# Kernel optimization log

Measured on AMD Instinct MI355X. Metric: run time of the kernel, lower is better.

Reference implementation:

```python
import jax, jax.numpy as jnp
import numpy as np

B, S, V, H, L, NH, DH, F, T = 256, 64, 21128, 768, 12, 12, 64, 3072, 11


def _layernorm(x, g, b):
    m = x.mean(-1, keepdims=True)
    v = ((x - m) ** 2).mean(-1, keepdims=True)
    return (x - m) / jnp.sqrt(v + 1e-12) * g + b


def setup_inputs():
    key = jax.random.key(0)
    ks = iter(jax.random.split(key, 24))
    std = 0.02
    w = lambda shape: jax.random.normal(next(ks), shape, jnp.float32) * std
    return {
        "input_ids": jax.random.randint(next(ks), (B, S), 0, V),
        "attention_mask": jnp.ones((B, S), jnp.int32),
        "label": jax.random.randint(next(ks), (B, S), 0, T),
        "word_emb": w((V, H)),
        "pos_emb": w((S, H)),
        "tok_emb": w((2, H)),
        "emb_ln_g": jnp.ones((H,), jnp.float32),
        "emb_ln_b": jnp.zeros((H,), jnp.float32),
        "Wqkv": w((L, H, 3 * H)),
        "bqkv": jnp.zeros((L, 3 * H), jnp.float32),
        "Wo": w((L, H, H)),
        "bo": jnp.zeros((L, H), jnp.float32),
        "ln1_g": jnp.ones((L, H), jnp.float32),
        "ln1_b": jnp.zeros((L, H), jnp.float32),
        "W1": w((L, H, F)),
        "b1": jnp.zeros((L, F), jnp.float32),
        "W2": w((L, F, H)),
        "b2": jnp.zeros((L, H), jnp.float32),
        "ln2_g": jnp.ones((L, H), jnp.float32),
        "ln2_b": jnp.zeros((L, H), jnp.float32),
        "fc_w": w((H, T)),
        "fc_b": jnp.zeros((T,), jnp.float32),
        "crf_start": w((T,)),
        "crf_end": w((T,)),
        "crf_trans": w((T, T)),
    }


def _encode(ids, mask, word_emb, pos_emb, tok_emb, eg, eb, layer_params):
    x = word_emb[ids] + pos_emb[None] + tok_emb[0][None, None]  # [B,S,H]
    x = _layernorm(x, eg, eb)
    bias = (1.0 - mask.astype(x.dtype))[:, None, None, :] * -1e9  # [B,1,1,S]

    def layer(x, p):
        Wqkv, bqkv, Wo, bo, g1, b1n, W1, b1, W2, b2, g2, b2n = p
        q, k, v = jnp.split(x @ Wqkv + bqkv, 3, axis=-1)
        sh = lambda t: t.reshape(B, S, NH, DH).transpose(0, 2, 1, 3)
        att = jax.nn.softmax(
            jnp.einsum("bhqd,bhkd->bhqk", sh(q), sh(k)) / jnp.sqrt(jnp.float32(DH)) + bias, -1
        )
        o = jnp.einsum("bhqk,bhkd->bhqd", att, sh(v)).transpose(0, 2, 1, 3).reshape(B, S, H)
        x = _layernorm(x + o @ Wo + bo, g1, b1n)
        h = jax.nn.gelu(x @ W1 + b1)
        x = _layernorm(x + h @ W2 + b2, g2, b2n)
        return x, None

    x, _ = jax.lax.scan(layer, x, layer_params)
    return x


def _crf_llh(em, tags, maskf, start, end, trans):
    # torchcrf log-likelihood, batch_first. em:[B,S,T] tags:[B,S] maskf:[B,S]
    bidx = jnp.arange(B)
    score = start[tags[:, 0]] + em[bidx, 0, tags[:, 0]]

    def num_step(s, xs):
        e_t, tp, tc, m = xs
        return s + (trans[tp, tc] + e_t[bidx, tc]) * m, None

    score, _ = jax.lax.scan(
        num_step, score,
        (em[:, 1:].transpose(1, 0, 2), tags[:, :-1].T, tags[:, 1:].T, maskf[:, 1:].T),
    )
    last_idx = maskf.sum(-1).astype(jnp.int32) - 1
    score = score + end[tags[bidx, last_idx]]

    alpha = start[None] + em[:, 0]  # [B,T]

    def den_step(a, xs):
        e_t, m = xs
        nxt = jax.scipy.special.logsumexp(a[:, :, None] + trans[None] + e_t[:, None, :], axis=1)
        return jnp.where(m[:, None] > 0, nxt, a), None

    alpha, _ = jax.lax.scan(den_step, alpha, (em[:, 1:].transpose(1, 0, 2), maskf[:, 1:].T))
    denom = jax.scipy.special.logsumexp(alpha + end[None], axis=1)
    return score - denom


def _viterbi(em, maskf, start, end, trans):
    bidx = jnp.arange(B)

    def step(s, xs):
        e_t, m = xs
        cand = s[:, :, None] + trans[None]  # [B,T_prev,T_cur]
        best_prev = jnp.argmax(cand, axis=1)  # [B,T]
        ns = jnp.max(cand, axis=1) + e_t
        return jnp.where(m[:, None] > 0, ns, s), best_prev

    score, hist = jax.lax.scan(
        step, start[None] + em[:, 0], (em[:, 1:].transpose(1, 0, 2), maskf[:, 1:].T)
    )  # hist: [S-1,B,T]
    last = jnp.argmax(score + end[None], axis=1)  # [B]

    def back(t, xs):
        h, m = xs
        nt = jnp.where(m > 0, h[bidx, t], t)
        return nt, nt

    _, prev_tags = jax.lax.scan(back, last, (hist, maskf[:, 1:].T), reverse=True)
    return jnp.concatenate([prev_tags.transpose(1, 0), last[:, None]], axis=1)  # [B,S]


def reference(input_ids, attention_mask, label, word_emb, pos_emb, tok_emb, emb_ln_g, emb_ln_b,
              Wqkv, bqkv, Wo, bo, ln1_g, ln1_b, W1, b1, W2, b2, ln2_g, ln2_b,
              fc_w, fc_b, crf_start, crf_end, crf_trans):
    lp = (Wqkv, bqkv, Wo, bo, ln1_g, ln1_b, W1, b1, W2, b2, ln2_g, ln2_b)
    x = _encode(input_ids, attention_mask, word_emb, pos_emb, tok_emb, emb_ln_g, emb_ln_b, lp)
    logits = x @ fc_w + fc_b  # [B,S,T]
    maskf = attention_mask.astype(jnp.float32)
    loss = -jnp.mean(_crf_llh(logits, label, maskf, crf_start, crf_end, crf_trans))
    pred = _viterbi(logits, maskf, crf_start, crf_end, crf_trans)
    return pred, loss
```

## Files before the change

### kernel.cpp

```cpp
#include <hip/hip_runtime.h>
#include <hip/hip_bf16.h>
#include <math.h>

namespace {

constexpr int B = 256, S = 64, H = 768, L = 12, NH = 12, F = 3072, T = 11;
constexpr int BS = B * S;
constexpr int RC = 8192;
constexpr int NCH = BS / RC;

typedef __attribute__((ext_vector_type(8))) short short8;
typedef __attribute__((ext_vector_type(4))) float f32x4;

__device__ __forceinline__ float gelu_tanh(float v) {
  float u = 0.7978845608028654f * (v + 0.044715f * v * v * v);
  u = fminf(fmaxf(u, -10.f), 10.f);
  float t = __expf(2.f * u);
  return 0.5f * v * (1.0f + (t - 1.f) / (t + 1.f));
}

__device__ __forceinline__ ushort f2bf(float v) {
  union { float f; unsigned u; } c; c.f = v;
  unsigned r = (c.u + 0x7fffu + ((c.u >> 16) & 1u)) >> 16;
  return (ushort)r;
}
__device__ __forceinline__ float bf2f(ushort u) {
  union { unsigned u; float f; } c; c.u = ((unsigned)u) << 16;
  return c.f;
}
__device__ __forceinline__ void split2(float v, ushort& hi, ushort& lo) {
  hi = f2bf(v);
  lo = f2bf(v - bf2f(hi));
}
__device__ __forceinline__ float join2(ushort hi, ushort lo) {
  return bf2f(hi) + bf2f(lo);
}
__device__ __forceinline__ int pcol(int c) { return ((c >> 5) << 6) + (c & 31); }

#define GLOAD_LDS16(gptr, ldsptr)                                                        \
  __builtin_amdgcn_global_load_lds((const __attribute__((address_space(1))) void*)(gptr), \
                                   (__attribute__((address_space(3))) void*)(ldsptr), 16, 0, 0)

template <int MODE>
__global__ __launch_bounds__(256, 3) void gemm_mfma(const ushort* __restrict__ A,
                                                    const ushort* __restrict__ Bw,
                                                    const float* __restrict__ bias,
                                                    float* __restrict__ outF,
                                                    ushort* __restrict__ outU,
                                                    int lda2, int ldb2, int ldc2,
                                                    int ldcF, int zStrideF, int ktiles) {
  __shared__ ushort sA[128 * 64];
  __shared__ ushort sB[128 * 64];
  const int tid = threadIdx.x;
  const int w = tid >> 6;
  const int lane = tid & 63;
  const int wm = w >> 1;
  const int wn = w & 1;

  const int gx = gridDim.x, gy = gridDim.y;
  const int flat = ((int)blockIdx.z * gy + blockIdx.y) * gx + blockIdx.x;
  const int q8 = (gx * gy * (int)gridDim.z) >> 3;
  const int swz = (flat & 7) * q8 + (flat >> 3);
  const int bx = swz % gx;
  const int by = (swz / gx) % gy;
  const int bz = swz / (gx * gy);
  const int bm = by * 128;
  const int bn = bx * 128;
  const int k0 = bz * ktiles * 64;

  const int srow = lane >> 3;
  const int sblk = (lane & 7) ^ srow;
  const ushort* Ab = A + (size_t)(bm + w * 32 + srow) * lda2 + k0 + sblk * 8;
  const ushort* Bb = Bw + (size_t)(bn + w * 32 + srow) * ldb2 + k0 + sblk * 8;

  const int fr = lane & 15;
  const int s7 = fr & 7;
  const int jb = lane >> 4;
  const int hOff = (jb ^ s7) << 3;
  const int lOff = ((4 + jb) ^ s7) << 3;

  f32x4 acc[4][4] = {};
  const int NT = ktiles;

  for (int t = 0; t < NT; ++t) {
#pragma unroll
    for (int c = 0; c < 4; ++c) {
      GLOAD_LDS16(Ab + (size_t)t * 64 + (size_t)(c * 8) * lda2, &sA[(w * 32 + c * 8) * 64]);
      GLOAD_LDS16(Bb + (size_t)t * 64 + (size_t)(c * 8) * ldb2, &sB[(w * 32 + c * 8) * 64]);
    }
    __syncthreads();

    short8 bh[4], bl[4];
#pragma unroll
    for (int ni = 0; ni < 4; ++ni) {
      const ushort* baseB = &sB[(wn * 64 + ni * 16 + fr) * 64];
      bh[ni] = *(const short8*)(baseB + hOff);
      bl[ni] = *(const short8*)(baseB + lOff);
    }
    __builtin_amdgcn_s_setprio(1);
#pragma unroll
    for (int mi = 0; mi < 4; ++mi) {
      const ushort* baseA = &sA[(wm * 64 + mi * 16 + fr) * 64];
      short8 ah = *(const short8*)(baseA + hOff);
      short8 al = *(const short8*)(baseA + lOff);
#pragma unroll
      for (int ni = 0; ni < 4; ++ni) {
        acc[mi][ni] = __builtin_amdgcn_mfma_f32_16x16x32_bf16(ah, bh[ni], acc[mi][ni], 0, 0, 0);
        acc[mi][ni] = __builtin_amdgcn_mfma_f32_16x16x32_bf16(ah, bl[ni], acc[mi][ni], 0, 0, 0);
        acc[mi][ni] = __builtin_amdgcn_mfma_f32_16x16x32_bf16(al, bh[ni], acc[mi][ni], 0, 0, 0);
      }
    }
    __builtin_amdgcn_s_setprio(0);
    __syncthreads();
  }

  const int erow = jb << 2;
#pragma unroll
  for (int ni = 0; ni < 4; ++ni) {
    const int col = bn + wn * 64 + ni * 16 + fr;
    const float bv = (MODE == 3) ? 0.f : bias[col];
    const int cb = pcol(col);
#pragma unroll
    for (int mi = 0; mi < 4; ++mi) {
#pragma unroll
      for (int e = 0; e < 4; ++e) {
        const int row = bm + wm * 64 + mi * 16 + erow + e;
        float v = acc[mi][ni][e] + bv;
        if (MODE == 1 || MODE == 2) {
          if (MODE == 1) v = gelu_tanh(v);
          ushort hi, lo;
          split2(v, hi, lo);
          outU[(size_t)row * ldc2 + cb] = hi;
          outU[(size_t)row * ldc2 + cb + 32] = lo;
        } else {
          outF[(size_t)bz * zStrideF + (size_t)row * ldcF + col] = v;
        }
      }
    }
  }
}

__global__ __launch_bounds__(256) void convert_w_t(const float* __restrict__ W,
                                                   ushort* __restrict__ WI, int K, int N) {
  __shared__ float tile[32][33];
  const int kb = blockIdx.y * 32, nb = blockIdx.x * 32;
  const int tr = threadIdx.x >> 5;
  const int tc = threadIdx.x & 31;
#pragma unroll
  for (int p = 0; p < 4; ++p) {
    int r = tr + p * 8;
    tile[r][tc] = W[(size_t)(kb + r) * N + nb + tc];
  }
  __syncthreads();
  const int kblk = kb >> 5;
#pragma unroll
  for (int p = 0; p < 4; ++p) {
    int n = tr + p * 8;
    float v = tile[tc][n];
    ushort hi, lo;
    split2(v, hi, lo);
    size_t o = (size_t)(nb + n) * (2 * K) + (size_t)kblk * 64 + tc;
    WI[o] = hi;
    WI[o + 32] = lo;
  }
}

__global__ __launch_bounds__(256) void attn_kernel(ushort* __restrict__ qkv,
                                                   const int* __restrict__ mask) {
  __shared__ float smem[64 * 64 + 64 * 66 + 64 * 64];
  float (*Qs)[64] = (float (*)[64])smem;
  float (*KsT)[66] = (float (*)[66])(smem + 64 * 64);
  float (*Vs)[64] = (float (*)[64])(smem + 64 * 64 + 64 * 66);
  float (*Ps)[65] = (float (*)[65])smem;

  const int bl = blockIdx.x / NH;
  const int hh = blockIdx.x % NH;
  const int tid = threadIdx.x;
  const int lane = tid & 63;
  const int w = tid >> 6;

  for (int i = 0; i < 16; ++i) {
    int idx = tid + i * 256;
    int r = idx >> 6, d = idx & 63;
    size_t rowb = (size_t)(bl * 64 + r) * 4608;
    int off = hh * 128 + pcol(d);
    Qs[r][d] = join2(qkv[rowb + off], qkv[rowb + off + 32]);
    KsT[d][r] = join2(qkv[rowb + 1536 + off], qkv[rowb + 1536 + off + 32]);
    Vs[r][d] = join2(qkv[rowb + 3072 + off], qkv[rowb + 3072 + off + 32]);
  }
  __syncthreads();

  float sc[16];
#pragma unroll
  for (int i = 0; i < 16; ++i) sc[i] = 0.f;
  for (int d = 0; d < 64; ++d) {
    float kv = KsT[d][lane];
#pragma unroll
    for (int i = 0; i < 16; ++i) sc[i] += Qs[w + 4 * i][d] * kv;
  }
  __syncthreads();
  float biask = (1.0f - (float)mask[bl * S + lane]) * -1e9f;
#pragma unroll
  for (int i = 0; i < 16; ++i) Ps[w + 4 * i][lane] = sc[i] * 0.125f + biask;
  __syncthreads();

  if (tid < 64) {
    int qr = tid;
    float mx = -1e30f;
    for (int k = 0; k < 64; ++k) mx = fmaxf(mx, Ps[qr][k]);
    float sum = 0.f;
    for (int k = 0; k < 64; ++k) {
      float e = expf(Ps[qr][k] - mx);
      Ps[qr][k] = e;
      sum += e;
    }
    float inv = 1.0f / sum;
    for (int k = 0; k < 64; ++k) Ps[qr][k] *= inv;
  }
  __syncthreads();

  float o[16];
#pragma unroll
  for (int i = 0; i < 16; ++i) o[i] = 0.f;
  for (int k = 0; k < 64; ++k) {
    float vv = Vs[k][lane];
#pragma unroll
    for (int i = 0; i < 16; ++i) o[i] += Ps[w + 4 * i][k] * vv;
  }
  const int ooff = hh * 128 + pcol(lane);
#pragma unroll
  for (int i = 0; i < 16; ++i) {
    int qr = w + 4 * i;
    size_t rowb = (size_t)(bl * 64 + qr) * 4608;
    ushort hi, lo;
    split2(o[i], hi, lo);
    qkv[rowb + ooff] = hi;
    qkv[rowb + ooff + 32] = lo;
  }
}

__global__ __launch_bounds__(256) void embed_ln_kernel(const int* __restrict__ ids,
                                                       const float* __restrict__ we,
                                                       const float* __restrict__ pe,
                                                       const float* __restrict__ te,
                                                       const float* __restrict__ g,
                                                       const float* __restrict__ bta,
                                                       ushort* __restrict__ xhl) {
  __shared__ float buf[H];
  __shared__ float red[256];
  const int row = blockIdx.x;
  const int s = row % S;
  const int tid = threadIdx.x;
  const int id = ids[row];
  float local = 0.f;
  for (int i = tid; i < H; i += 256) {
    float v = we[(size_t)id * H + i] + pe[(size_t)s * H + i] + te[i];
    buf[i] = v;
    local += v;
  }
  red[tid] = local;
  __syncthreads();
  for (int st = 128; st > 0; st >>= 1) {
    if (tid < st) red[tid] += red[tid + st];
    __syncthreads();
  }
  float mean = red[0] * (1.0f / H);
  __syncthreads();
  float ls = 0.f;
  for (int i = tid; i < H; i += 256) {
    float d = buf[i] - mean;
    ls += d * d;
  }
  red[tid] = ls;
  __syncthreads();
  for (int st = 128; st > 0; st >>= 1) {
    if (tid < st) red[tid] += red[tid + st];
    __syncthreads();
  }
  float inv = 1.0f / sqrtf(red[0] * (1.0f / H) + 1e-12f);
  for (int i = tid; i < H; i += 256) {
    float o = (buf[i] - mean) * inv * g[i] + bta[i];
    int cb = pcol(i);
    ushort hi, lo;
    split2(o, hi, lo);
    xhl[(size_t)row * (2 * H) + cb] = hi;
    xhl[(size_t)row * (2 * H) + cb + 32] = lo;
  }
}

__global__ __launch_bounds__(256) void add_ln_kernel(ushort* __restrict__ xhl,
                                                     const float* __restrict__ pz0,
                                                     const float* __restrict__ pz1,
                                                     int prs,
                                                     const float* __restrict__ biasv,
                                                     const float* __restrict__ g,
                                                     const float* __restrict__ bta) {
  __shared__ float buf[H];
  __shared__ float red[256];
  const size_t row = blockIdx.x;
  const int tid = threadIdx.x;
  float local = 0.f;
  for (int i = tid; i < H; i += 256) {
    int cb = pcol(i);
    float v = join2(xhl[row * (2 * H) + cb], xhl[row * (2 * H) + cb + 32]) +
              ((pz0[row * (size_t)prs + i] + pz1[row * (size_t)prs + i]) + biasv[i]);
    buf[i] = v;
    local += v;
  }
  red[tid] = local;
  __syncthreads();
  for (int st = 128; st > 0; st >>= 1) {
    if (tid < st) red[tid] += red[tid + st];
    __syncthreads();
  }
  float mean = red[0] * (1.0f / H);
  __syncthreads();
  float ls = 0.f;
  for (int i = tid; i < H; i += 256) {
    float d = buf[i] - mean;
    ls += d * d;
  }
  red[tid] = ls;
  __syncthreads();
  for (int st = 128; st > 0; st >>= 1) {
    if (tid < st) red[tid] += red[tid + st];
    __syncthreads();
  }
  float inv = 1.0f / sqrtf(red[0] * (1.0f / H) + 1e-12f);
  for (int i = tid; i < H; i += 256) {
    float o = (buf[i] - mean) * inv * g[i] + bta[i];
    int cb = pcol(i);
    ushort hi, lo;
    split2(o, hi, lo);
    xhl[row * (2 * H) + cb] = hi;
    xhl[row * (2 * H) + cb + 32] = lo;
  }
}

__global__ __launch_bounds__(256) void fc_kernel(const ushort* __restrict__ xhl,
                                                 const float* __restrict__ w,
                                                 const float* __restrict__ bias,
                                                 float* __restrict__ logits) {
  __shared__ float xs[H];
  const size_t row = blockIdx.x;
  const int tid = threadIdx.x;
  for (int i = tid; i < H; i += 256) {
    int cb = pcol(i);
    xs[i] = join2(xhl[row * (2 * H) + cb], xhl[row * (2 * H) + cb + 32]);
  }
  __syncthreads();
  const int j = tid >> 4, l = tid & 15;
  if (j < T) {
    float s = 0.f;
    for (int k = l; k < H; k += 16) s += xs[k] * w[(size_t)k * T + j];
#pragma unroll
    for (int d = 8; d > 0; d >>= 1) s += __shfl_down(s, d, 16);
    if (l == 0) logits[row * T + j] = s + bias[j];
  }
}

__global__ __launch_bounds__(64) void crf_llh_kernel(const float* __restrict__ em,
                                                     const int* __restrict__ label,
                                                     const int* __restrict__ mask,
                                                     const float* __restrict__ start,
                                                     const float* __restrict__ endw,
                                                     const float* __restrict__ trans,
                                                     float* __restrict__ llh) {
  const int b = blockIdx.x;
  const int c = threadIdx.x;
  __shared__ float alpha[T];
  __shared__ float tr[T][T];
  for (int i = c; i < T * T; i += 64) tr[i / T][i % T] = trans[i];
  if (c < T) alpha[c] = start[c] + em[(size_t)b * S * T + c];
  __syncthreads();
  for (int s = 1; s < S; ++s) {
    float a = 0.f;
    if (c < T) {
      float mx = -1e30f;
      for (int p = 0; p < T; ++p) mx = fmaxf(mx, alpha[p] + tr[p][c]);
      float sum = 0.f;
      for (int p = 0; p < T; ++p) sum += expf(alpha[p] + tr[p][c] - mx);
      a = mx + logf(sum) + em[((size_t)b * S + s) * T + c];
    }
    __syncthreads();
    if (c < T) {
      float m = (float)mask[b * S + s];
      alpha[c] = (m > 0.f) ? a : alpha[c];
    }
    __syncthreads();
  }
  if (c == 0) {
    float mx = -1e30f;
    for (int p = 0; p < T; ++p) mx = fmaxf(mx, alpha[p] + endw[p]);
    float sum = 0.f;
    for (int p = 0; p < T; ++p) sum += expf(alpha[p] + endw[p] - mx);
    float denom = mx + logf(sum);

    int t0 = label[b * S];
    float score = start[t0] + em[(size_t)b * S * T + t0];
    int prev = t0;
    for (int s = 1; s < S; ++s) {
      int tc = label[b * S + s];
      float m = (float)mask[b * S + s];
      score += (tr[prev][tc] + em[((size_t)b * S + s) * T + tc]) * m;
      prev = tc;
    }
    int msum = 0;
    for (int s = 0; s < S; ++s) msum += mask[b * S + s];
    score += endw[label[b * S + (msum - 1)]];
    llh[b] = score - denom;
  }
}

__global__ __launch_bounds__(256) void loss_kernel(const float* __restrict__ llh,
                                                   float* __restrict__ out) {
  __shared__ float red[256];
  const int tid = threadIdx.x;
  red[tid] = llh[tid];
  __syncthreads();
  for (int st = 128; st > 0; st >>= 1) {
    if (tid < st) red[tid] += red[tid + st];
    __syncthreads();
  }
  if (tid == 0) out[BS] = -red[0] * (1.0f / B);
}

__global__ __launch_bounds__(64) void viterbi_kernel(const float* __restrict__ em,
                                                     const int* __restrict__ mask,
                                                     const float* __restrict__ start,
                                                     const float* __restrict__ endw,
                                                     const float* __restrict__ trans,
                                                     float* __restrict__ pred) {
  const int b = blockIdx.x;
  const int c = threadIdx.x;
  __shared__ float sc[T];
  __shared__ float tr[T][T];
  __shared__ int hist[S - 1][T];
  for (int i = c; i < T * T; i += 64) tr[i / T][i % T] = trans[i];
  if (c < T) sc[c] = start[c] + em[(size_t)b * S * T + c];
  __syncthreads();
  for (int s = 1; s < S; ++s) {
    float bestv = -1e30f;
    int bestp = 0;
    if (c < T) {
      for (int p = 0; p < T; ++p) {
        float v = sc[p] + tr[p][c];
        if (v > bestv) { bestv = v; bestp = p; }
      }
      hist[s - 1][c] = bestp;
    }
    __syncthreads();
    if (c < T) {
      float m = (float)mask[b * S + s];
      sc[c] = (m > 0.f) ? (bestv + em[((size_t)b * S + s) * T + c]) : sc[c];
    }
    __syncthreads();
  }
  if (c == 0) {
    float bv = -1e30f;
    int last = 0;
    for (int p = 0; p < T; ++p) {
      float v = sc[p] + endw[p];
      if (v > bv) { bv = v; last = p; }
    }
    pred[b * S + (S - 1)] = (float)last;
    int t = last;
    for (int hs = S - 2; hs >= 0; --hs) {
      if (mask[b * S + hs + 1] > 0) t = hist[hs][t];
      pred[b * S + hs] = (float)t;
    }
  }
}

}

extern "C" void kernel_launch(void* const* d_in, const int* in_sizes, int n_in,
                              void* d_out, int out_size, void* d_ws, size_t ws_size,
                              hipStream_t stream) {
  (void)in_sizes; (void)n_in; (void)out_size; (void)ws_size;
  const int* input_ids = (const int*)d_in[0];
  const int* attn_mask = (const int*)d_in[1];
  const int* label = (const int*)d_in[2];
  const float* word_emb = (const float*)d_in[3];
  const float* pos_emb = (const float*)d_in[4];
  const float* tok_emb = (const float*)d_in[5];
  const float* eg = (const float*)d_in[6];
  const float* ebt = (const float*)d_in[7];
  const float* Wqkv = (const float*)d_in[8];
  const float* bqkv = (const float*)d_in[9];
  const float* Wo = (const float*)d_in[10];
  const float* bo = (const float*)d_in[11];
  const float* ln1g = (const float*)d_in[12];
  const float* ln1b = (const float*)d_in[13];
  const float* W1 = (const float*)d_in[14];
  const float* b1 = (const float*)d_in[15];
  const float* W2 = (const float*)d_in[16];
  const float* b2 = (const float*)d_in[17];
  const float* ln2g = (const float*)d_in[18];
  const float* ln2b = (const float*)d_in[19];
  const float* fc_w = (const float*)d_in[20];
  const float* fc_b = (const float*)d_in[21];
  const float* crf_start = (const float*)d_in[22];
  const float* crf_end = (const float*)d_in[23];
  const float* crf_trans = (const float*)d_in[24];
  float* out = (float*)d_out;

  char* p = (char*)d_ws;
  ushort* xhl = (ushort*)p;    p += (size_t)BS * 2 * H * 2;
  ushort* wQ = (ushort*)p;     p += (size_t)3 * H * 2 * H * 2;
  ushort* wO = (ushort*)p;     p += (size_t)H * 2 * H * 2;
  ushort* wF1 = (ushort*)p;    p += (size_t)F * 2 * H * 2;
  ushort* wF2 = (ushort*)p;    p += (size_t)H * 2 * F * 2;
  char* big = p;               p += (size_t)BS * 3 * H * 4;
  float* logits = (float*)p;   p += (size_t)BS * T * 4;
  float* llh = (float*)p;      p += (size_t)B * 4;
  ushort* qkvP = (ushort*)big;
  float* qf = (float*)big;
  ushort* hU = (ushort*)big;
  float* pf = (float*)(big + (size_t)RC * F * 4);

  embed_ln_kernel<<<BS, 256, 0, stream>>>(input_ids, word_emb, pos_emb, tok_emb, eg, ebt, xhl);

  for (int l = 0; l < L; ++l) {
    const float* wqkv_l = Wqkv + (size_t)l * H * 3 * H;
    const float* bqkv_l = bqkv + (size_t)l * 3 * H;
    const float* wo_l = Wo + (size_t)l * H * H;
    const float* bo_l = bo + (size_t)l * H;
    const float* g1 = ln1g + (size_t)l * H;
    const float* be1 = ln1b + (size_t)l * H;
    const float* w1_l = W1 + (size_t)l * H * F;
    const float* b1_l = b1 + (size_t)l * F;
    const float* w2_l = W2 + (size_t)l * F * H;
    const float* b2_l = b2 + (size_t)l * H;
    const float* g2 = ln2g + (size_t)l * H;
    const float* be2 = ln2b + (size_t)l * H;

    convert_w_t<<<dim3(3 * H / 32, H / 32), 256, 0, stream>>>(wqkv_l, wQ, H, 3 * H);
    convert_w_t<<<dim3(H / 32, H / 32), 256, 0, stream>>>(wo_l, wO, H, H);
    convert_w_t<<<dim3(F / 32, H / 32), 256, 0, stream>>>(w1_l, wF1, H, F);
    convert_w_t<<<dim3(H / 32, F / 32), 256, 0, stream>>>(w2_l, wF2, F, H);

    gemm_mfma<2><<<dim3(3 * H / 128, BS / 128, 1), 256, 0, stream>>>(
        xhl, wQ, bqkv_l, nullptr, qkvP, 2 * H, 2 * H, 2 * 3 * H, 0, 0, H / 32);
    attn_kernel<<<B * NH, 256, 0, stream>>>(qkvP, attn_mask);
    gemm_mfma<3><<<dim3(H / 128, BS / 128, 2), 256, 0, stream>>>(
        qkvP, wO, nullptr, qf + H, nullptr, 2 * 3 * H, 2 * H, 0, 3 * H, H, H / 64);
    add_ln_kernel<<<BS, 256, 0, stream>>>(xhl, qf + H, qf + 2 * H, 3 * H, bo_l, g1, be1);

    for (int ch = 0; ch < NCH; ++ch) {
      gemm_mfma<1><<<dim3(F / 128, RC / 128, 1), 256, 0, stream>>>(
          xhl + (size_t)ch * RC * 2 * H, wF1, b1_l, nullptr, hU, 2 * H, 2 * H, 2 * F,
          0, 0, H / 32);
      gemm_mfma<3><<<dim3(H / 128, RC / 128, 2), 256, 0, stream>>>(
          hU, wF2, nullptr, pf, nullptr, 2 * F, 2 * F, 0, H, RC * H, F / 64);
      add_ln_kernel<<<RC, 256, 0, stream>>>(xhl + (size_t)ch * RC * 2 * H, pf,
                                            pf + (size_t)RC * H, H, b2_l, g2, be2);
    }
  }

  fc_kernel<<<BS, 256, 0, stream>>>(xhl, fc_w, fc_b, logits);
  crf_llh_kernel<<<B, 64, 0, stream>>>(logits, label, attn_mask, crf_start, crf_end, crf_trans, llh);
  loss_kernel<<<1, 256, 0, stream>>>(llh, out);
  viterbi_kernel<<<B, 64, 0, stream>>>(logits, attn_mask, crf_start, crf_end, crf_trans, out);
}
```

Measured before the change: 10.53 ms.

## Vectorize packed hi/lo loads in attention, layernorm and fc; drop split-K for Wo

Attention staging, add+layernorm and fc row loading now read the packed bf16 hi/lo layout with 16-byte short8 vector loads instead of scalar ushort accesses. Layernorm keeps its row values in registers rather than a shared buffer, and only 96 of the 256 threads do work. The Wo projection GEMM switches from a 2-way split-K to a single full-K pass, so the following add_ln reads one partial instead of two. The aim is fewer memory transactions and less partial-sum traffic, at the cost of fewer Wo GEMM blocks and idle threads in layernorm.

```diff
diff --git a/kernel.cpp b/kernel.cpp
--- a/kernel.cpp
+++ b/kernel.cpp
@@ -34,6 +34,9 @@
 }
 __device__ __forceinline__ float join2(ushort hi, ushort lo) {
   return bf2f(hi) + bf2f(lo);
+}
+__device__ __forceinline__ float join2s(short hi, short lo) {
+  return join2((ushort)hi, (ushort)lo);
 }
 __device__ __forceinline__ int pcol(int c) { return ((c >> 5) << 6) + (c & 31); }
 
@@ -179,14 +182,25 @@
   const int lane = tid & 63;
   const int w = tid >> 6;
 
-  for (int i = 0; i < 16; ++i) {
-    int idx = tid + i * 256;
-    int r = idx >> 6, d = idx & 63;
+#pragma unroll
+  for (int it = 0; it < 2; ++it) {
+    int item = tid + it * 256;
+    int r = item >> 3, gq = item & 7;
     size_t rowb = (size_t)(bl * 64 + r) * 4608;
-    int off = hh * 128 + pcol(d);
-    Qs[r][d] = join2(qkv[rowb + off], qkv[rowb + off + 32]);
-    KsT[d][r] = join2(qkv[rowb + 1536 + off], qkv[rowb + 1536 + off + 32]);
-    Vs[r][d] = join2(qkv[rowb + 3072 + off], qkv[rowb + 3072 + off + 32]);
+    int off = hh * 128 + (gq >> 2) * 64 + (gq & 3) * 8;
+    short8 qh = *(const short8*)(qkv + rowb + off);
+    short8 ql = *(const short8*)(qkv + rowb + off + 32);
+    short8 kh = *(const short8*)(qkv + rowb + 1536 + off);
+    short8 kl = *(const short8*)(qkv + rowb + 1536 + off + 32);
+    short8 vh = *(const short8*)(qkv + rowb + 3072 + off);
+    short8 vl = *(const short8*)(qkv + rowb + 3072 + off + 32);
+#pragma unroll
+    for (int j = 0; j < 8; ++j) {
+      int d = gq * 8 + j;
+      Qs[r][d] = join2s(qh[j], ql[j]);
+      KsT[d][r] = join2s(kh[j], kl[j]);
+      Vs[r][d] = join2s(vh[j], vl[j]);
+    }
   }
   __syncthreads();
 
@@ -288,6 +302,7 @@
   }
 }
 
+template <int NP>
 __global__ __launch_bounds__(256) void add_ln_kernel(ushort* __restrict__ xhl,
                                                      const float* __restrict__ pz0,
                                                      const float* __restrict__ pz1,
@@ -295,17 +310,37 @@
                                                      const float* __restrict__ biasv,
                                                      const float* __restrict__ g,
                                                      const float* __restrict__ bta) {
-  __shared__ float buf[H];
   __shared__ float red[256];
   const size_t row = blockIdx.x;
   const int tid = threadIdx.x;
+  float v[8];
   float local = 0.f;
-  for (int i = tid; i < H; i += 256) {
-    int cb = pcol(i);
-    float v = join2(xhl[row * (2 * H) + cb], xhl[row * (2 * H) + cb + 32]) +
-              ((pz0[row * (size_t)prs + i] + pz1[row * (size_t)prs + i]) + biasv[i]);
-    buf[i] = v;
-    local += v;
+  const int gq = tid;
+  const int c0 = gq * 8;
+  ushort* base = xhl + row * (2 * H) + (gq >> 2) * 64 + (gq & 3) * 8;
+  if (tid < 96) {
+    short8 hi = *(const short8*)(base);
+    short8 lo = *(const short8*)(base + 32);
+    f32x4 p0a = *(const f32x4*)(pz0 + row * (size_t)prs + c0);
+    f32x4 p0b = *(const f32x4*)(pz0 + row * (size_t)prs + c0 + 4);
+    f32x4 ba = *(const f32x4*)(biasv + c0);
+    f32x4 bb = *(const f32x4*)(biasv + c0 + 4);
+#pragma unroll
+    for (int j = 0; j < 4; ++j) {
+      v[j] = join2s(hi[j], lo[j]) + (p0a[j] + ba[j]);
+      v[4 + j] = join2s(hi[4 + j], lo[4 + j]) + (p0b[j] + bb[j]);
+    }
+    if (NP == 2) {
+      f32x4 p1a = *(const f32x4*)(pz1 + row * (size_t)prs + c0);
+      f32x4 p1b = *(const f32x4*)(pz1 + row * (size_t)prs + c0 + 4);
+#pragma unroll
+      for (int j = 0; j < 4; ++j) {
+        v[j] += p1a[j];
+        v[4 + j] += p1b[j];
+      }
+    }
+#pragma unroll
+    for (int j = 0; j < 8; ++j) local += v[j];
   }
   red[tid] = local;
   __syncthreads();
@@ -316,9 +351,12 @@
   float mean = red[0] * (1.0f / H);
   __syncthreads();
   float ls = 0.f;
-  for (int i = tid; i < H; i += 256) {
-    float d = buf[i] - mean;
-    ls += d * d;
+  if (tid < 96) {
+#pragma unroll
+    for (int j = 0; j < 8; ++j) {
+      float d = v[j] - mean;
+      ls += d * d;
+    }
   }
   red[tid] = ls;
   __syncthreads();
@@ -327,13 +365,24 @@
     __syncthreads();
   }
   float inv = 1.0f / sqrtf(red[0] * (1.0f / H) + 1e-12f);
-  for (int i = tid; i < H; i += 256) {
-    float o = (buf[i] - mean) * inv * g[i] + bta[i];
-    int cb = pcol(i);
-    ushort hi, lo;
-    split2(o, hi, lo);
-    xhl[row * (2 * H) + cb] = hi;
-    xhl[row * (2 * H) + cb + 32] = lo;
+  if (tid < 96) {
+    f32x4 ga = *(const f32x4*)(g + c0);
+    f32x4 gb = *(const f32x4*)(g + c0 + 4);
+    f32x4 ta = *(const f32x4*)(bta + c0);
+    f32x4 tb = *(const f32x4*)(bta + c0 + 4);
+    short8 ho, lo8;
+#pragma unroll
+    for (int j = 0; j < 4; ++j) {
+      float o = (v[j] - mean) * inv * ga[j] + ta[j];
+      ushort hi, lo;
+      split2(o, hi, lo);
+      ho[j] = (short)hi; lo8[j] = (short)lo;
+      o = (v[4 + j] - mean) * inv * gb[j] + tb[j];
+      split2(o, hi, lo);
+      ho[4 + j] = (short)hi; lo8[4 + j] = (short)lo;
+    }
+    *(short8*)(base) = ho;
+    *(short8*)(base + 32) = lo8;
   }
 }
 
@@ -344,9 +393,12 @@
   __shared__ float xs[H];
   const size_t row = blockIdx.x;
   const int tid = threadIdx.x;
-  for (int i = tid; i < H; i += 256) {
-    int cb = pcol(i);
-    xs[i] = join2(xhl[row * (2 * H) + cb], xhl[row * (2 * H) + cb + 32]);
+  if (tid < 96) {
+    const ushort* base = xhl + row * (2 * H) + (tid >> 2) * 64 + (tid & 3) * 8;
+    short8 hi = *(const short8*)(base);
+    short8 lo = *(const short8*)(base + 32);
+#pragma unroll
+    for (int j = 0; j < 8; ++j) xs[tid * 8 + j] = join2s(hi[j], lo[j]);
   }
   __syncthreads();
   const int j = tid >> 4, l = tid & 15;
@@ -543,9 +595,9 @@
     gemm_mfma<2><<<dim3(3 * H / 128, BS / 128, 1), 256, 0, stream>>>(
         xhl, wQ, bqkv_l, nullptr, qkvP, 2 * H, 2 * H, 2 * 3 * H, 0, 0, H / 32);
     attn_kernel<<<B * NH, 256, 0, stream>>>(qkvP, attn_mask);
-    gemm_mfma<3><<<dim3(H / 128, BS / 128, 2), 256, 0, stream>>>(
-        qkvP, wO, nullptr, qf + H, nullptr, 2 * 3 * H, 2 * H, 0, 3 * H, H, H / 64);
-    add_ln_kernel<<<BS, 256, 0, stream>>>(xhl, qf + H, qf + 2 * H, 3 * H, bo_l, g1, be1);
+    gemm_mfma<3><<<dim3(H / 128, BS / 128, 1), 256, 0, stream>>>(
+        qkvP, wO, nullptr, qf + H, nullptr, 2 * 3 * H, 2 * H, 0, 3 * H, 0, H / 32);
+    add_ln_kernel<1><<<BS, 256, 0, stream>>>(xhl, qf + H, nullptr, 3 * H, bo_l, g1, be1);
 
     for (int ch = 0; ch < NCH; ++ch) {
       gemm_mfma<1><<<dim3(F / 128, RC / 128, 1), 256, 0, stream>>>(
@@ -553,8 +605,8 @@
           0, 0, H / 32);
       gemm_mfma<3><<<dim3(H / 128, RC / 128, 2), 256, 0, stream>>>(
           hU, wF2, nullptr, pf, nullptr, 2 * F, 2 * F, 0, H, RC * H, F / 64);
-      add_ln_kernel<<<RC, 256, 0, stream>>>(xhl + (size_t)ch * RC * 2 * H, pf,
-                                            pf + (size_t)RC * H, H, b2_l, g2, be2);
+      add_ln_kernel<2><<<RC, 256, 0, stream>>>(xhl + (size_t)ch * RC * 2 * H, pf,
+                                               pf + (size_t)RC * H, H, b2_l, g2, be2);
     }
   }
 
```

Result: faster. 10.21 ms (-3.0%).
